# Performance work log

Hardware: AMD Instinct MI355X
Metric: run time of the kernel (lower is better)

Reference implementation:

```python
import jax, jax.numpy as jnp
import numpy as np

N_FEAT = 64
O_FEAT = 64
REDUCTION = 16


def conv2d(x, w, pad):
    # x: NCHW, w: OIHW
    return jax.lax.conv_general_dilated(
        x, w, window_strides=(1, 1), padding=[(pad, pad), (pad, pad)],
        dimension_numbers=('NCHW', 'OIHW', 'NCHW'))


def bwt(x):
    # Haar-like wavelet decompose: [B,C,H,W] -> [B,8C,H/2,W/2]
    x01 = x[:, :, 0::2, :] / 2
    x02 = x[:, :, 1::2, :] / 2
    x1 = x01[:, :, :, 0::2]
    x2 = x02[:, :, :, 0::2]
    x3 = x01[:, :, :, 1::2]
    x4 = x02[:, :, :, 1::2]
    x_LL = x1 + x2 + x3 + x4
    x_HL = -x1 - x2 + x3 + x4
    x_LH = -x1 + x2 - x3 + x4
    x_HH = x1 - x2 - x3 + x4
    x_HD = x1 + x2 - x3 - x4
    x_LV = -x1 + x2 + x3 - x4
    x_LD = x1 - x2 + x3 - x4
    x_HV = -x1 - x2 - x3 - x4
    return jnp.concatenate((x_LL, x_HL, x_LH, x_HH, x_HD, x_LV, x_LD, x_HV), axis=1)


def ibwt(x):
    # [B,8C,h,w] -> [B,C,2h,2w]
    B, C8, h, w = x.shape
    C = C8 // 8
    xs = [x[:, i * C:(i + 1) * C] / 2 for i in range(8)]
    x1, x2, x3, x4, x5, x6, x7, x8 = xs
    a00 = x1 - x2 - x3 + x4 + x5 - x6 + x7 - x8  # h[0::2, 0::2]
    a10 = x1 - x2 + x3 - x4 - x5 + x6 - x7 + x8  # h[1::2, 0::2]
    a01 = x1 + x2 - x3 - x4 - x5 - x6 + x7 + x8  # h[0::2, 1::2]
    a11 = x1 + x2 + x3 + x4 + x5 + x6 + x7 + x8  # h[1::2, 1::2]
    # interleave columns then rows
    even_rows = jnp.stack([a00, a01], axis=-1).reshape(B, C, h, 2 * w)
    odd_rows = jnp.stack([a10, a11], axis=-1).reshape(B, C, h, 2 * w)
    return jnp.stack([even_rows, odd_rows], axis=-2).reshape(B, C, 2 * h, 2 * w)


def sal(x, w_sal):
    max_pool = jnp.max(x, axis=1, keepdims=True)
    avg_pool = jnp.mean(x, axis=1, keepdims=True)
    channel_pool = jnp.concatenate([max_pool, avg_pool], axis=1)
    y = jax.nn.sigmoid(conv2d(channel_pool, w_sal, pad=2))
    return x * y


def cal(x, w_ca1, w_ca2):
    y = jnp.mean(x, axis=(2, 3), keepdims=True)  # adaptive avg pool to 1x1
    y = jax.nn.relu(conv2d(y, w_ca1, pad=0))
    y = jax.nn.sigmoid(conv2d(y, w_ca2, pad=0))
    return x * y


def setup_inputs() -> dict:
    key = jax.random.key(0)
    ks = jax.random.split(key, 10)
    n, o, r = N_FEAT, O_FEAT, REDUCTION
    s = 0.05
    return {
        'x': jax.random.normal(ks[0], (4, n, 256, 256), dtype=jnp.float32),
        'w_body1': jax.random.normal(ks[1], (n, 8 * n, 3, 3), dtype=jnp.float32) * s,
        'w_body2': jax.random.normal(ks[2], (8 * n, n, 3, 3), dtype=jnp.float32) * s,
        'w_sal': jax.random.normal(ks[3], (1, 2, 5, 5), dtype=jnp.float32) * s,
        'w_ca1': jax.random.normal(ks[4], (8 * n // r, 8 * n, 1, 1), dtype=jnp.float32) * s,
        'w_ca2': jax.random.normal(ks[5], (8 * n, 8 * n // r, 1, 1), dtype=jnp.float32) * s,
        'w_1x1': jax.random.normal(ks[6], (8 * n, 8 * n, 1, 1), dtype=jnp.float32) * s,
        'w_3x3': jax.random.normal(ks[7], (o, n, 3, 3), dtype=jnp.float32) * s,
        'w_final': jax.random.normal(ks[8], (o, n, 1, 1), dtype=jnp.float32) * s,
    }


def reference(x, w_body1, w_body2, w_sal, w_ca1, w_ca2, w_1x1, w_3x3, w_final):
    residual = x
    x_bwt = bwt(x)                               # [B, 8n, H/2, W/2]
    res = conv2d(x_bwt, w_body1, pad=1)          # body: conv-act-conv
    res = jax.nn.relu(res)
    res = conv2d(res, w_body2, pad=1)
    res = sal(res, w_sal)
    res = cal(res, w_ca1, w_ca2)
    res = conv2d(res, w_1x1, pad=0) + x_bwt
    wavelet_path = ibwt(res)                     # [B, n, H, W]
    out = jax.nn.relu(conv2d(wavelet_path, w_3x3, pad=1))
    out = out + conv2d(residual, w_final, pad=0)
    return out
```

## Files before the change

kernel.cpp:

```cpp
#include <hip/hip_runtime.h>
#include <hip/hip_bf16.h>

typedef __hip_bfloat16 bf16;
using short8  = __attribute__((ext_vector_type(8))) short;
using floatx4 = __attribute__((ext_vector_type(4))) float;

__device__ __forceinline__ float b2f(bf16 v) { return __bfloat162float(v); }
__device__ __forceinline__ bf16 f2b(float v) { return __float2bfloat16(v); }
__device__ __forceinline__ float s2f(short s) {
    return __uint_as_float(((unsigned)(unsigned short)s) << 16);
}

constexpr int Bz = 4, H = 256, W = 256, Hh = 128, Wh = 128, C8 = 512;
constexpr int HWh = Hh * Wh;
constexpr int HWf = H * W;
constexpr int ICP = 40;

template<int OC, int IC>
__global__ __launch_bounds__(256) void prep_wr(const float* __restrict__ w, bf16* __restrict__ wr) {
    int idx = blockIdx.x * 256 + threadIdx.x;
    if (idx >= 9 * OC * IC) return;
    int ic = idx & (IC - 1);
    int oc = (idx / IC) & (OC - 1);
    int tap = idx / (IC * OC);
    wr[idx] = f2b(w[(oc * IC + ic) * 9 + tap]);
}

__global__ __launch_bounds__(256) void prep_wfr(const float* __restrict__ wf, bf16* __restrict__ wfr) {
    int idx = blockIdx.x * 256 + threadIdx.x;
    wfr[idx] = f2b(wf[idx]);
}

__global__ __launch_bounds__(256) void prep_w1s(const float* __restrict__ w1,
                                                const float* __restrict__ scale,
                                                bf16* __restrict__ w1s) {
    int idx = blockIdx.x * 256 + threadIdx.x;
    int ic = idx & 511, oc = (idx >> 9) & 511, b = idx >> 18;
    w1s[idx] = f2b(w1[oc * 512 + ic] * scale[b * 512 + ic]);
}

__global__ __launch_bounds__(256) void bwt_nhwc(const float* __restrict__ x, bf16* __restrict__ A) {
    int idx = blockIdx.x * 256 + threadIdx.x;
    int c = idx & 63;
    int j = (idx >> 6) & 127;
    int i = (idx >> 13) & 127;
    int b = idx >> 20;
    const float* xp = x + ((size_t)(b * 64 + c) * H + 2 * i) * W + 2 * j;
    float2 ev = *(const float2*)xp;
    float2 od = *(const float2*)(xp + W);
    float x1 = ev.x * 0.5f, x3 = ev.y * 0.5f, x2 = od.x * 0.5f, x4 = od.y * 0.5f;
    float v[8];
    v[0] =  x1 + x2 + x3 + x4;
    v[1] = -x1 - x2 + x3 + x4;
    v[2] = -x1 + x2 - x3 + x4;
    v[3] =  x1 - x2 - x3 + x4;
    v[4] =  x1 + x2 - x3 - x4;
    v[5] = -x1 + x2 + x3 - x4;
    v[6] =  x1 - x2 + x3 - x4;
    v[7] = -x1 - x2 - x3 - x4;
    size_t base = (size_t)(idx >> 6) * 512 + c;
    #pragma unroll
    for (int k = 0; k < 8; k++)
        A[base + k * 64] = f2b(v[k]);
}

template<int IC, int OC, int HW, int TR, bool RELU>
__global__ __launch_bounds__(256, 2) void conv3x3_mfma(const bf16* __restrict__ in,
                                                       const bf16* __restrict__ wr,
                                                       bf16* __restrict__ out) {
    constexpr int MT = TR / 4;
    __shared__ bf16 sIn[(TR + 2) * 18 * ICP];
    __shared__ bf16 sW3[3 * 64 * ICP];

    const int tilesX = HW / 16;
    int tX = (blockIdx.x % tilesX) * 16;
    int tY = (blockIdx.x / tilesX) * TR;
    int oBase = blockIdx.y * 64;
    int b = blockIdx.z;
    int tid = threadIdx.x;
    int lane = tid & 63, wid = tid >> 6;
    int m = lane & 15, quad = lane >> 4;

    floatx4 acc[MT][4];
    #pragma unroll
    for (int i = 0; i < MT; i++)
        #pragma unroll
        for (int j = 0; j < 4; j++)
            acc[i][j] = (floatx4){0.f, 0.f, 0.f, 0.f};

    const bf16* inB = in + (size_t)b * HW * HW * IC;

    for (int ic0 = 0; ic0 < IC; ic0 += 32) {
        __syncthreads();
        for (int e = tid; e < (TR + 2) * 18 * 4; e += 256) {
            int q = e & 3, cell = e >> 2;
            int r = cell / 18, c = cell - r * 18;
            int gr = tY + r - 1, gc = tX + c - 1;
            short8 v = {0, 0, 0, 0, 0, 0, 0, 0};
            if (gr >= 0 && gr < HW && gc >= 0 && gc < HW)
                v = *(const short8*)(inB + (size_t)(gr * HW + gc) * IC + ic0 + q * 8);
            *(short8*)(sIn + cell * ICP + q * 8) = v;
        }
        for (int dy = 0; dy < 3; dy++) {
            if (dy) __syncthreads();
            for (int e = tid; e < 768; e += 256) {
                int q = e & 3, row = e >> 2;
                int dxl = row >> 6, oc = row & 63;
                int tap = dy * 3 + dxl;
                short8 v = *(const short8*)(wr + (size_t)(tap * OC + oBase + oc) * IC + ic0 + q * 8);
                *(short8*)(sW3 + row * ICP + q * 8) = v;
            }
            __syncthreads();
            #pragma unroll
            for (int dx = 0; dx < 3; dx++) {
                short8 bfr[4];
                #pragma unroll
                for (int nt = 0; nt < 4; nt++)
                    bfr[nt] = *(const short8*)(sW3 + (dx * 64 + nt * 16 + m) * ICP + quad * 8);
                #pragma unroll
                for (int mt = 0; mt < MT; mt++) {
                    int r = wid * MT + mt;
                    short8 afr = *(const short8*)(sIn + ((r + dy) * 18 + m + dx) * ICP + quad * 8);
                    #pragma unroll
                    for (int nt = 0; nt < 4; nt++)
                        acc[mt][nt] = __builtin_amdgcn_mfma_f32_16x16x32_bf16(afr, bfr[nt], acc[mt][nt], 0, 0, 0);
                }
            }
        }
    }
    #pragma unroll
    for (int mt = 0; mt < MT; mt++) {
        int row = tY + wid * MT + mt;
        #pragma unroll
        for (int nt = 0; nt < 4; nt++) {
            int oc = oBase + nt * 16 + m;
            #pragma unroll
            for (int reg = 0; reg < 4; reg++) {
                int col = tX + quad * 4 + reg;
                float v = acc[mt][nt][reg];
                if (RELU) v = fmaxf(v, 0.f);
                out[((size_t)(b * HW + row) * HW + col) * OC + oc] = f2b(v);
            }
        }
    }
}

__global__ __launch_bounds__(256, 2) void conv1x1_mfma(const bf16* __restrict__ t3,
                                                       const bf16* __restrict__ w1s,
                                                       bf16* __restrict__ A) {
    __shared__ bf16 sX[256 * ICP];
    __shared__ bf16 sW1[64 * ICP];
    int p0 = blockIdx.x * 256;
    int oBase = blockIdx.y * 64;
    int b = blockIdx.z;
    int tid = threadIdx.x;
    int lane = tid & 63, wid = tid >> 6;
    int m = lane & 15, quad = lane >> 4;
    const bf16* wB = w1s + (size_t)b * 512 * 512;
    const bf16* tB = t3 + ((size_t)b << 14) * 512;

    floatx4 acc[4][4];
    #pragma unroll
    for (int i = 0; i < 4; i++)
        #pragma unroll
        for (int j = 0; j < 4; j++)
            acc[i][j] = (floatx4){0.f, 0.f, 0.f, 0.f};

    for (int ic0 = 0; ic0 < 512; ic0 += 32) {
        __syncthreads();
        #pragma unroll
        for (int k = 0; k < 4; k++) {
            int e = tid + k * 256;
            int q = e & 3, p = e >> 2;
            *(short8*)(sX + p * ICP + q * 8) =
                *(const short8*)(tB + (size_t)(p0 + p) * 512 + ic0 + q * 8);
        }
        {
            int q = tid & 3, oc = tid >> 2;
            *(short8*)(sW1 + oc * ICP + q * 8) =
                *(const short8*)(wB + (size_t)(oBase + oc) * 512 + ic0 + q * 8);
        }
        __syncthreads();
        short8 bfr[4];
        #pragma unroll
        for (int nt = 0; nt < 4; nt++)
            bfr[nt] = *(const short8*)(sW1 + (nt * 16 + m) * ICP + quad * 8);
        #pragma unroll
        for (int mt = 0; mt < 4; mt++) {
            short8 afr = *(const short8*)(sX + ((wid * 4 + mt) * 16 + m) * ICP + quad * 8);
            #pragma unroll
            for (int nt = 0; nt < 4; nt++)
                acc[mt][nt] = __builtin_amdgcn_mfma_f32_16x16x32_bf16(afr, bfr[nt], acc[mt][nt], 0, 0, 0);
        }
    }
    bf16* AB = A + ((size_t)b << 14) * 512;
    #pragma unroll
    for (int mt = 0; mt < 4; mt++) {
        #pragma unroll
        for (int nt = 0; nt < 4; nt++) {
            int oc = oBase + nt * 16 + m;
            #pragma unroll
            for (int reg = 0; reg < 4; reg++) {
                int p = p0 + (wid * 4 + mt) * 16 + quad * 4 + reg;
                size_t a = (size_t)p * 512 + oc;
                AB[a] = f2b(acc[mt][nt][reg] + b2f(AB[a]));
            }
        }
    }
}

__global__ __launch_bounds__(256) void sal_pool(const bf16* __restrict__ t2, float* __restrict__ pool) {
    int pix = blockIdx.x * 4 + (threadIdx.x >> 6);
    int lane = threadIdx.x & 63;
    short8 v = *(const short8*)(t2 + (size_t)pix * 512 + lane * 8);
    float mx = -1e30f, sm = 0.f;
    #pragma unroll
    for (int i = 0; i < 8; i++) {
        float f = s2f(v[i]);
        mx = fmaxf(mx, f);
        sm += f;
    }
    #pragma unroll
    for (int off = 32; off > 0; off >>= 1) {
        mx = fmaxf(mx, __shfl_xor(mx, off));
        sm += __shfl_xor(sm, off);
    }
    if (lane == 0) {
        int b = pix >> 14, px = pix & (HWh - 1);
        pool[((size_t)(b * 2) << 14) + px] = mx;
        pool[((size_t)(b * 2 + 1) << 14) + px] = sm * (1.f / 512.f);
    }
}

__global__ __launch_bounds__(256) void sal_conv(const float* __restrict__ pool,
                                                const float* __restrict__ wsal,
                                                float* __restrict__ smap) {
    int p = blockIdx.x * 256 + threadIdx.x;
    int b = p >> 14, px = p & (HWh - 1);
    int iy = px >> 7, ix = px & 127;
    float acc = 0.f;
    #pragma unroll
    for (int ch = 0; ch < 2; ch++)
        #pragma unroll
        for (int dy = 0; dy < 5; dy++)
            #pragma unroll
            for (int dx = 0; dx < 5; dx++) {
                int gy = iy + dy - 2, gx = ix + dx - 2;
                if (gy >= 0 && gy < Hh && gx >= 0 && gx < Wh)
                    acc += pool[((size_t)(b * 2 + ch) << 14) + gy * Wh + gx] *
                           wsal[ch * 25 + dy * 5 + dx];
            }
    smap[p] = 1.f / (1.f + expf(-acc));
}

__global__ __launch_bounds__(256) void sal_mul_sum(bf16* __restrict__ t2,
                                                   const float* __restrict__ smap,
                                                   float* __restrict__ chsum) {
    int b = blockIdx.y;
    int p0 = blockIdx.x * 32;
    int t = threadIdx.x;
    float s0 = 0.f, s1 = 0.f;
    bf16* tB = t2 + ((size_t)b << 14) * 512;
    #pragma unroll 4
    for (int k = 0; k < 32; k++) {
        int pix = p0 + k;
        float sc = smap[(b << 14) + pix];
        size_t base = (size_t)pix * 512 + 2 * t;
        float f0 = b2f(tB[base]) * sc;
        float f1 = b2f(tB[base + 1]) * sc;
        tB[base] = f2b(f0);
        tB[base + 1] = f2b(f1);
        s0 += f0; s1 += f1;
    }
    atomicAdd(&chsum[b * 512 + 2 * t], s0);
    atomicAdd(&chsum[b * 512 + 2 * t + 1], s1);
}

__global__ __launch_bounds__(512) void cal_kernel(const float* __restrict__ chsum,
                                                  const float* __restrict__ wca1,
                                                  const float* __restrict__ wca2,
                                                  float* __restrict__ scale) {
    int b = blockIdx.x;
    __shared__ float sMean[512];
    __shared__ float sH[32];
    sMean[threadIdx.x] = chsum[b * C8 + threadIdx.x] * (1.f / 16384.f);
    __syncthreads();
    if (threadIdx.x < 32) {
        float a = 0.f;
        for (int cc = 0; cc < 512; cc++)
            a += wca1[threadIdx.x * 512 + cc] * sMean[cc];
        sH[threadIdx.x] = fmaxf(a, 0.f);
    }
    __syncthreads();
    float a = 0.f;
    #pragma unroll
    for (int j = 0; j < 32; j++)
        a += wca2[threadIdx.x * 32 + j] * sH[j];
    scale[b * C8 + threadIdx.x] = 1.f / (1.f + expf(-a));
}

__global__ __launch_bounds__(256) void ibwt_nhwc(const bf16* __restrict__ A, bf16* __restrict__ E) {
    int idx = blockIdx.x * 256 + threadIdx.x;
    int c = idx & 63;
    int j = (idx >> 6) & 127;
    int i = (idx >> 13) & 127;
    int b = idx >> 20;
    size_t base = (size_t)(idx >> 6) * 512 + c;
    float xs[8];
    #pragma unroll
    for (int k = 0; k < 8; k++)
        xs[k] = b2f(A[base + k * 64]) * 0.5f;
    float a00 = xs[0] - xs[1] - xs[2] + xs[3] + xs[4] - xs[5] + xs[6] - xs[7];
    float a10 = xs[0] - xs[1] + xs[2] - xs[3] - xs[4] + xs[5] - xs[6] + xs[7];
    float a01 = xs[0] + xs[1] - xs[2] - xs[3] - xs[4] - xs[5] + xs[6] + xs[7];
    float a11 = xs[0] + xs[1] + xs[2] + xs[3] + xs[4] + xs[5] + xs[6] + xs[7];
    bf16* Ep = E + ((size_t)((b * H + 2 * i) * W + 2 * j)) * 64 + c;
    Ep[0]          = f2b(a00);
    Ep[64]         = f2b(a01);
    Ep[W * 64]     = f2b(a10);
    Ep[W * 64 + 64] = f2b(a11);
}

__global__ __launch_bounds__(256, 2) void final_mfma(const bf16* __restrict__ E,
                                                     const bf16* __restrict__ wr3,
                                                     const float* __restrict__ x,
                                                     const bf16* __restrict__ wfr,
                                                     float* __restrict__ out) {
    __shared__ bf16 sIn[18 * 18 * ICP];
    __shared__ bf16 sW3[3 * 64 * ICP];
    const int tilesX = W / 16;
    int tX = (blockIdx.x % tilesX) * 16;
    int tY = (blockIdx.x / tilesX) * 16;
    int b = blockIdx.z;
    int tid = threadIdx.x;
    int lane = tid & 63, wid = tid >> 6;
    int m = lane & 15, quad = lane >> 4;

    floatx4 acc[4][4];
    #pragma unroll
    for (int i = 0; i < 4; i++)
        #pragma unroll
        for (int j = 0; j < 4; j++)
            acc[i][j] = (floatx4){0.f, 0.f, 0.f, 0.f};

    const bf16* inB = E + (size_t)b * HWf * 64;
    for (int ic0 = 0; ic0 < 64; ic0 += 32) {
        __syncthreads();
        for (int e = tid; e < 18 * 18 * 4; e += 256) {
            int q = e & 3, cell = e >> 2;
            int r = cell / 18, c = cell - r * 18;
            int gr = tY + r - 1, gc = tX + c - 1;
            short8 v = {0, 0, 0, 0, 0, 0, 0, 0};
            if (gr >= 0 && gr < H && gc >= 0 && gc < W)
                v = *(const short8*)(inB + (size_t)(gr * W + gc) * 64 + ic0 + q * 8);
            *(short8*)(sIn + cell * ICP + q * 8) = v;
        }
        for (int dy = 0; dy < 3; dy++) {
            if (dy) __syncthreads();
            for (int e = tid; e < 768; e += 256) {
                int q = e & 3, row = e >> 2;
                int dxl = row >> 6, oc = row & 63;
                int tap = dy * 3 + dxl;
                short8 v = *(const short8*)(wr3 + (size_t)(tap * 64 + oc) * 64 + ic0 + q * 8);
                *(short8*)(sW3 + row * ICP + q * 8) = v;
            }
            __syncthreads();
            #pragma unroll
            for (int dx = 0; dx < 3; dx++) {
                short8 bfr[4];
                #pragma unroll
                for (int nt = 0; nt < 4; nt++)
                    bfr[nt] = *(const short8*)(sW3 + (dx * 64 + nt * 16 + m) * ICP + quad * 8);
                #pragma unroll
                for (int mt = 0; mt < 4; mt++) {
                    int r = wid * 4 + mt;
                    short8 afr = *(const short8*)(sIn + ((r + dy) * 18 + m + dx) * ICP + quad * 8);
                    #pragma unroll
                    for (int nt = 0; nt < 4; nt++)
                        acc[mt][nt] = __builtin_amdgcn_mfma_f32_16x16x32_bf16(afr, bfr[nt], acc[mt][nt], 0, 0, 0);
                }
            }
        }
    }
    #pragma unroll
    for (int i = 0; i < 4; i++)
        #pragma unroll
        for (int j = 0; j < 4; j++)
            #pragma unroll
            for (int r = 0; r < 4; r++)
                acc[i][j][r] = fmaxf(acc[i][j][r], 0.f);

    for (int icc = 0; icc < 64; icc += 32) {
        __syncthreads();
        for (int e = tid; e < 2048; e += 256) {
            int c4 = e & 3, r = (e >> 2) & 15, ic = e >> 6;
            float4 v = *(const float4*)(x + ((size_t)(b * 64 + icc + ic) * H + tY + r) * W + tX + c4 * 4);
            bf16* dst = sIn + ((r + 1) * 18 + c4 * 4 + 1) * ICP + ic;
            dst[0]       = f2b(v.x);
            dst[ICP]     = f2b(v.y);
            dst[2 * ICP] = f2b(v.z);
            dst[3 * ICP] = f2b(v.w);
        }
        {
            int q = tid & 3, oc = tid >> 2;
            *(short8*)(sW3 + (64 + oc) * ICP + q * 8) =
                *(const short8*)(wfr + oc * 64 + icc + q * 8);
        }
        __syncthreads();
        short8 bfr[4];
        #pragma unroll
        for (int nt = 0; nt < 4; nt++)
            bfr[nt] = *(const short8*)(sW3 + (64 + nt * 16 + m) * ICP + quad * 8);
        #pragma unroll
        for (int mt = 0; mt < 4; mt++) {
            int r = wid * 4 + mt;
            short8 afr = *(const short8*)(sIn + ((r + 1) * 18 + m + 1) * ICP + quad * 8);
            #pragma unroll
            for (int nt = 0; nt < 4; nt++)
                acc[mt][nt] = __builtin_amdgcn_mfma_f32_16x16x32_bf16(afr, bfr[nt], acc[mt][nt], 0, 0, 0);
        }
    }
    #pragma unroll
    for (int mt = 0; mt < 4; mt++) {
        int gr = tY + wid * 4 + mt;
        #pragma unroll
        for (int nt = 0; nt < 4; nt++) {
            int oc = nt * 16 + m;
            *(floatx4*)(out + ((size_t)(b * 64 + oc) * H + gr) * W + tX + quad * 4) = acc[mt][nt];
        }
    }
}

extern "C" void kernel_launch(void* const* d_in, const int* in_sizes, int n_in,
                              void* d_out, int out_size, void* d_ws, size_t ws_size,
                              hipStream_t stream) {
    const float* x       = (const float*)d_in[0];
    const float* w_body1 = (const float*)d_in[1];
    const float* w_body2 = (const float*)d_in[2];
    const float* w_sal   = (const float*)d_in[3];
    const float* w_ca1   = (const float*)d_in[4];
    const float* w_ca2   = (const float*)d_in[5];
    const float* w_1x1   = (const float*)d_in[6];
    const float* w_3x3   = (const float*)d_in[7];
    const float* w_final = (const float*)d_in[8];

    char* ws = (char*)d_ws;
    bf16*  A     = (bf16*)(ws + 0);
    bf16*  T2    = (bf16*)(ws + 67108864);
    bf16*  T1    = (bf16*)(ws + 134217728);
    float* pool  = (float*)(ws + 134217728);
    float* smap  = (float*)(ws + 134742016);
    float* chsum = (float*)(ws + 135004160);
    float* scale = (float*)(ws + 135012352);
    bf16*  w1s   = (bf16*)(ws + 135020544);
    bf16*  wr3   = (bf16*)(ws + 137117696);
    bf16*  wfr   = (bf16*)(ws + 137191424);
    bf16*  E     = T2;
    bf16*  wr1   = (bf16*)d_out;
    bf16*  wr2   = (bf16*)((char*)d_out + 589824);

    prep_wr<64, 512><<<1152, 256, 0, stream>>>(w_body1, wr1);
    prep_wr<512, 64><<<1152, 256, 0, stream>>>(w_body2, wr2);
    bwt_nhwc<<<16384, 256, 0, stream>>>(x, A);
    conv3x3_mfma<512, 64, 128, 8, true ><<<dim3(128, 1, 4), 256, 0, stream>>>(A, wr1, T1);
    conv3x3_mfma<64, 512, 128, 16, false><<<dim3(64, 8, 4), 256, 0, stream>>>(T1, wr2, T2);
    sal_pool<<<16384, 256, 0, stream>>>(T2, pool);
    sal_conv<<<256, 256, 0, stream>>>(pool, w_sal, smap);
    hipMemsetAsync(chsum, 0, 4 * 512 * sizeof(float), stream);
    sal_mul_sum<<<dim3(512, 4), 256, 0, stream>>>(T2, smap, chsum);
    cal_kernel<<<4, 512, 0, stream>>>(chsum, w_ca1, w_ca2, scale);
    prep_w1s<<<4096, 256, 0, stream>>>(w_1x1, scale, w1s);
    prep_wr<64, 64><<<144, 256, 0, stream>>>(w_3x3, wr3);
    prep_wfr<<<16, 256, 0, stream>>>(w_final, wfr);
    conv1x1_mfma<<<dim3(64, 8, 4), 256, 0, stream>>>(T2, w1s, A);
    ibwt_nhwc<<<16384, 256, 0, stream>>>(A, E);
    final_mfma<<<dim3(256, 1, 4), 256, 0, stream>>>(E, wr3, x, wfr, (float*)d_out);
}
```

Measured before the change: 521.9 us.

## Fuse spatial-attention scaling into 1x1 conv, restage weights, tile bwt via LDS

The spatial-attention multiply no longer writes back into T2. sal_wsum only accumulates the weighted channel sums, and the smap scaling is applied while T2 is staged into shared memory inside conv1x1, which also widens its output tile to 128 channels. The 3x3 convs and final kernel load all nine tap weights per input-channel chunk with one barrier instead of three, and the first conv uses 16-row tiles with launch bound 1. bwt now stages coalesced float4 reads through LDS, rounding x to bf16 before the transform. This cuts one full read-modify-write pass over T2 and some synchronisation, at the cost of more LDS and registers, lower occupancy and fewer blocks for conv1.

```diff
diff --git a/kernel.cpp b/kernel.cpp
--- a/kernel.cpp
+++ b/kernel.cpp
@@ -10,8 +10,12 @@
 __device__ __forceinline__ float s2f(short s) {
     return __uint_as_float(((unsigned)(unsigned short)s) << 16);
 }
-
-constexpr int Bz = 4, H = 256, W = 256, Hh = 128, Wh = 128, C8 = 512;
+__device__ __forceinline__ unsigned short fbits(float v) {
+    bf16 b = f2b(v);
+    return *(unsigned short*)&b;
+}
+
+constexpr int H = 256, W = 256, Hh = 128, Wh = 128, C8 = 512;
 constexpr int HWh = Hh * Wh;
 constexpr int HWf = H * W;
 constexpr int ICP = 40;
@@ -39,51 +43,68 @@
     w1s[idx] = f2b(w1[oc * 512 + ic] * scale[b * 512 + ic]);
 }
 
-__global__ __launch_bounds__(256) void bwt_nhwc(const float* __restrict__ x, bf16* __restrict__ A) {
-    int idx = blockIdx.x * 256 + threadIdx.x;
-    int c = idx & 63;
-    int j = (idx >> 6) & 127;
-    int i = (idx >> 13) & 127;
-    int b = idx >> 20;
-    const float* xp = x + ((size_t)(b * 64 + c) * H + 2 * i) * W + 2 * j;
-    float2 ev = *(const float2*)xp;
-    float2 od = *(const float2*)(xp + W);
-    float x1 = ev.x * 0.5f, x3 = ev.y * 0.5f, x2 = od.x * 0.5f, x4 = od.y * 0.5f;
-    float v[8];
-    v[0] =  x1 + x2 + x3 + x4;
-    v[1] = -x1 - x2 + x3 + x4;
-    v[2] = -x1 + x2 - x3 + x4;
-    v[3] =  x1 - x2 - x3 + x4;
-    v[4] =  x1 + x2 - x3 - x4;
-    v[5] = -x1 + x2 + x3 - x4;
-    v[6] =  x1 - x2 + x3 - x4;
-    v[7] = -x1 - x2 - x3 - x4;
-    size_t base = (size_t)(idx >> 6) * 512 + c;
-    #pragma unroll
-    for (int k = 0; k < 8; k++)
-        A[base + k * 64] = f2b(v[k]);
-}
-
-template<int IC, int OC, int HW, int TR, bool RELU>
-__global__ __launch_bounds__(256, 2) void conv3x3_mfma(const bf16* __restrict__ in,
-                                                       const bf16* __restrict__ wr,
-                                                       bf16* __restrict__ out) {
-    constexpr int MT = TR / 4;
-    __shared__ bf16 sIn[(TR + 2) * 18 * ICP];
-    __shared__ bf16 sW3[3 * 64 * ICP];
+constexpr int XROW = 130;
+__global__ __launch_bounds__(256, 2) void bwt_nhwc(const float* __restrict__ x, bf16* __restrict__ A) {
+    __shared__ unsigned short sX[2 * 64 * XROW];
+    int bx = blockIdx.x;
+    int i = bx >> 1, j0 = (bx & 1) * 64;
+    int b = blockIdx.z;
+    int tid = threadIdx.x;
+    for (int k = 0; k < 16; k++) {
+        int e = tid + k * 256;
+        int w4 = e & 31, r = (e >> 5) & 1, c = e >> 6;
+        float4 v = *(const float4*)(x + (((size_t)(b * 64 + c) * H + 2 * i + r) * W) + j0 * 2 + w4 * 4);
+        unsigned lo = ((unsigned)fbits(v.y) << 16) | fbits(v.x);
+        unsigned hi = ((unsigned)fbits(v.w) << 16) | fbits(v.z);
+        unsigned short* dst = sX + (r * 64 + c) * XROW + w4 * 4;
+        *(unsigned*)(dst) = lo;
+        *(unsigned*)(dst + 2) = hi;
+    }
+    __syncthreads();
+    int c = tid & 63, wid = tid >> 6;
+    for (int k = 0; k < 16; k++) {
+        int jr = wid * 16 + k;
+        unsigned ev = *(const unsigned*)(sX + c * XROW + jr * 2);
+        unsigned od = *(const unsigned*)(sX + (64 + c) * XROW + jr * 2);
+        float x1 = s2f((short)(ev & 0xffff)) * 0.5f;
+        float x3 = s2f((short)(ev >> 16)) * 0.5f;
+        float x2 = s2f((short)(od & 0xffff)) * 0.5f;
+        float x4 = s2f((short)(od >> 16)) * 0.5f;
+        float v[8];
+        v[0] =  x1 + x2 + x3 + x4;
+        v[1] = -x1 - x2 + x3 + x4;
+        v[2] = -x1 + x2 - x3 + x4;
+        v[3] =  x1 - x2 - x3 + x4;
+        v[4] =  x1 + x2 - x3 - x4;
+        v[5] = -x1 + x2 + x3 - x4;
+        v[6] =  x1 - x2 + x3 - x4;
+        v[7] = -x1 - x2 - x3 - x4;
+        size_t base = ((size_t)((b * Hh + i) * Wh) + j0 + jr) * 512 + c;
+        #pragma unroll
+        for (int band = 0; band < 8; band++)
+            A[base + band * 64] = f2b(v[band]);
+    }
+}
+
+template<int IC, int OC, int HW, bool RELU, int MINW>
+__global__ __launch_bounds__(256, MINW) void conv3x3_mfma(const bf16* __restrict__ in,
+                                                          const bf16* __restrict__ wr,
+                                                          bf16* __restrict__ out) {
+    __shared__ bf16 sIn[18 * 18 * ICP];
+    __shared__ bf16 sW9[9 * 64 * ICP];
 
     const int tilesX = HW / 16;
     int tX = (blockIdx.x % tilesX) * 16;
-    int tY = (blockIdx.x / tilesX) * TR;
+    int tY = (blockIdx.x / tilesX) * 16;
     int oBase = blockIdx.y * 64;
     int b = blockIdx.z;
     int tid = threadIdx.x;
     int lane = tid & 63, wid = tid >> 6;
     int m = lane & 15, quad = lane >> 4;
 
-    floatx4 acc[MT][4];
-    #pragma unroll
-    for (int i = 0; i < MT; i++)
+    floatx4 acc[4][4];
+    #pragma unroll
+    for (int i = 0; i < 4; i++)
         #pragma unroll
         for (int j = 0; j < 4; j++)
             acc[i][j] = (floatx4){0.f, 0.f, 0.f, 0.f};
@@ -92,7 +113,7 @@
 
     for (int ic0 = 0; ic0 < IC; ic0 += 32) {
         __syncthreads();
-        for (int e = tid; e < (TR + 2) * 18 * 4; e += 256) {
+        for (int e = tid; e < 18 * 18 * 4; e += 256) {
             int q = e & 3, cell = e >> 2;
             int r = cell / 18, c = cell - r * 18;
             int gr = tY + r - 1, gc = tX + c - 1;
@@ -101,25 +122,24 @@
                 v = *(const short8*)(inB + (size_t)(gr * HW + gc) * IC + ic0 + q * 8);
             *(short8*)(sIn + cell * ICP + q * 8) = v;
         }
+        for (int e = tid; e < 2304; e += 256) {
+            int q = e & 3, row = e >> 2;
+            int tap = row >> 6, oc = row & 63;
+            short8 v = *(const short8*)(wr + (size_t)(tap * OC + oBase + oc) * IC + ic0 + q * 8);
+            *(short8*)(sW9 + row * ICP + q * 8) = v;
+        }
+        __syncthreads();
+        #pragma unroll
         for (int dy = 0; dy < 3; dy++) {
-            if (dy) __syncthreads();
-            for (int e = tid; e < 768; e += 256) {
-                int q = e & 3, row = e >> 2;
-                int dxl = row >> 6, oc = row & 63;
-                int tap = dy * 3 + dxl;
-                short8 v = *(const short8*)(wr + (size_t)(tap * OC + oBase + oc) * IC + ic0 + q * 8);
-                *(short8*)(sW3 + row * ICP + q * 8) = v;
-            }
-            __syncthreads();
             #pragma unroll
             for (int dx = 0; dx < 3; dx++) {
                 short8 bfr[4];
                 #pragma unroll
                 for (int nt = 0; nt < 4; nt++)
-                    bfr[nt] = *(const short8*)(sW3 + (dx * 64 + nt * 16 + m) * ICP + quad * 8);
+                    bfr[nt] = *(const short8*)(sW9 + ((dy * 3 + dx) * 64 + nt * 16 + m) * ICP + quad * 8);
                 #pragma unroll
-                for (int mt = 0; mt < MT; mt++) {
-                    int r = wid * MT + mt;
+                for (int mt = 0; mt < 4; mt++) {
+                    int r = wid * 4 + mt;
                     short8 afr = *(const short8*)(sIn + ((r + dy) * 18 + m + dx) * ICP + quad * 8);
                     #pragma unroll
                     for (int nt = 0; nt < 4; nt++)
@@ -129,8 +149,8 @@
         }
     }
     #pragma unroll
-    for (int mt = 0; mt < MT; mt++) {
-        int row = tY + wid * MT + mt;
+    for (int mt = 0; mt < 4; mt++) {
+        int row = tY + wid * 4 + mt;
         #pragma unroll
         for (int nt = 0; nt < 4; nt++) {
             int oc = oBase + nt * 16 + m;
@@ -146,24 +166,26 @@
 }
 
 __global__ __launch_bounds__(256, 2) void conv1x1_mfma(const bf16* __restrict__ t3,
+                                                       const float* __restrict__ smap,
                                                        const bf16* __restrict__ w1s,
                                                        bf16* __restrict__ A) {
     __shared__ bf16 sX[256 * ICP];
-    __shared__ bf16 sW1[64 * ICP];
+    __shared__ bf16 sW1[128 * ICP];
     int p0 = blockIdx.x * 256;
-    int oBase = blockIdx.y * 64;
+    int oBase = blockIdx.y * 128;
     int b = blockIdx.z;
     int tid = threadIdx.x;
     int lane = tid & 63, wid = tid >> 6;
     int m = lane & 15, quad = lane >> 4;
     const bf16* wB = w1s + (size_t)b * 512 * 512;
     const bf16* tB = t3 + ((size_t)b << 14) * 512;
-
-    floatx4 acc[4][4];
+    const float* sm = smap + (b << 14);
+
+    floatx4 acc[4][8];
     #pragma unroll
     for (int i = 0; i < 4; i++)
         #pragma unroll
-        for (int j = 0; j < 4; j++)
+        for (int j = 0; j < 8; j++)
             acc[i][j] = (floatx4){0.f, 0.f, 0.f, 0.f};
 
     for (int ic0 = 0; ic0 < 512; ic0 += 32) {
@@ -172,24 +194,31 @@
         for (int k = 0; k < 4; k++) {
             int e = tid + k * 256;
             int q = e & 3, p = e >> 2;
-            *(short8*)(sX + p * ICP + q * 8) =
-                *(const short8*)(tB + (size_t)(p0 + p) * 512 + ic0 + q * 8);
-        }
-        {
-            int q = tid & 3, oc = tid >> 2;
+            float sc = sm[p0 + p];
+            short8 v = *(const short8*)(tB + (size_t)(p0 + p) * 512 + ic0 + q * 8);
+            short8 o;
+            #pragma unroll
+            for (int t = 0; t < 8; t++)
+                o[t] = (short)fbits(s2f(v[t]) * sc);
+            *(short8*)(sX + p * ICP + q * 8) = o;
+        }
+        #pragma unroll
+        for (int k = 0; k < 2; k++) {
+            int e = tid + k * 256;
+            int q = e & 3, oc = e >> 2;
             *(short8*)(sW1 + oc * ICP + q * 8) =
                 *(const short8*)(wB + (size_t)(oBase + oc) * 512 + ic0 + q * 8);
         }
         __syncthreads();
-        short8 bfr[4];
-        #pragma unroll
-        for (int nt = 0; nt < 4; nt++)
+        short8 bfr[8];
+        #pragma unroll
+        for (int nt = 0; nt < 8; nt++)
             bfr[nt] = *(const short8*)(sW1 + (nt * 16 + m) * ICP + quad * 8);
         #pragma unroll
         for (int mt = 0; mt < 4; mt++) {
             short8 afr = *(const short8*)(sX + ((wid * 4 + mt) * 16 + m) * ICP + quad * 8);
             #pragma unroll
-            for (int nt = 0; nt < 4; nt++)
+            for (int nt = 0; nt < 8; nt++)
                 acc[mt][nt] = __builtin_amdgcn_mfma_f32_16x16x32_bf16(afr, bfr[nt], acc[mt][nt], 0, 0, 0);
         }
     }
@@ -197,11 +226,11 @@
     #pragma unroll
     for (int mt = 0; mt < 4; mt++) {
         #pragma unroll
-        for (int nt = 0; nt < 4; nt++) {
+        for (int nt = 0; nt < 8; nt++) {
             int oc = oBase + nt * 16 + m;
             #pragma unroll
             for (int reg = 0; reg < 4; reg++) {
-                int p = p0 + (wid * 4 + mt) * 16 + quad * 4 + reg;
+                int p = p0 + wid * 64 + mt * 16 + quad * 4 + reg;
                 size_t a = (size_t)p * 512 + oc;
                 AB[a] = f2b(acc[mt][nt][reg] + b2f(AB[a]));
             }
@@ -253,24 +282,21 @@
     smap[p] = 1.f / (1.f + expf(-acc));
 }
 
-__global__ __launch_bounds__(256) void sal_mul_sum(bf16* __restrict__ t2,
-                                                   const float* __restrict__ smap,
-                                                   float* __restrict__ chsum) {
+__global__ __launch_bounds__(256) void sal_wsum(const bf16* __restrict__ t2,
+                                                const float* __restrict__ smap,
+                                                float* __restrict__ chsum) {
     int b = blockIdx.y;
     int p0 = blockIdx.x * 32;
     int t = threadIdx.x;
     float s0 = 0.f, s1 = 0.f;
-    bf16* tB = t2 + ((size_t)b << 14) * 512;
+    const bf16* tB = t2 + ((size_t)b << 14) * 512;
     #pragma unroll 4
     for (int k = 0; k < 32; k++) {
         int pix = p0 + k;
         float sc = smap[(b << 14) + pix];
-        size_t base = (size_t)pix * 512 + 2 * t;
-        float f0 = b2f(tB[base]) * sc;
-        float f1 = b2f(tB[base + 1]) * sc;
-        tB[base] = f2b(f0);
-        tB[base + 1] = f2b(f1);
-        s0 += f0; s1 += f1;
+        unsigned v = *(const unsigned*)(tB + (size_t)pix * 512 + 2 * t);
+        s0 += s2f((short)(v & 0xffff)) * sc;
+        s1 += s2f((short)(v >> 16)) * sc;
     }
     atomicAdd(&chsum[b * 512 + 2 * t], s0);
     atomicAdd(&chsum[b * 512 + 2 * t + 1], s1);
@@ -315,9 +341,9 @@
     float a01 = xs[0] + xs[1] - xs[2] - xs[3] - xs[4] - xs[5] + xs[6] + xs[7];
     float a11 = xs[0] + xs[1] + xs[2] + xs[3] + xs[4] + xs[5] + xs[6] + xs[7];
     bf16* Ep = E + ((size_t)((b * H + 2 * i) * W + 2 * j)) * 64 + c;
-    Ep[0]          = f2b(a00);
-    Ep[64]         = f2b(a01);
-    Ep[W * 64]     = f2b(a10);
+    Ep[0]           = f2b(a00);
+    Ep[64]          = f2b(a01);
+    Ep[W * 64]      = f2b(a10);
     Ep[W * 64 + 64] = f2b(a11);
 }
 
@@ -327,7 +353,7 @@
                                                      const bf16* __restrict__ wfr,
                                                      float* __restrict__ out) {
     __shared__ bf16 sIn[18 * 18 * ICP];
-    __shared__ bf16 sW3[3 * 64 * ICP];
+    __shared__ bf16 sW9[9 * 64 * ICP];
     const int tilesX = W / 16;
     int tX = (blockIdx.x % tilesX) * 16;
     int tY = (blockIdx.x / tilesX) * 16;
@@ -355,22 +381,21 @@
                 v = *(const short8*)(inB + (size_t)(gr * W + gc) * 64 + ic0 + q * 8);
             *(short8*)(sIn + cell * ICP + q * 8) = v;
         }
+        for (int e = tid; e < 2304; e += 256) {
+            int q = e & 3, row = e >> 2;
+            int tap = row >> 6, oc = row & 63;
+            short8 v = *(const short8*)(wr3 + (size_t)(tap * 64 + oc) * 64 + ic0 + q * 8);
+            *(short8*)(sW9 + row * ICP + q * 8) = v;
+        }
+        __syncthreads();
+        #pragma unroll
         for (int dy = 0; dy < 3; dy++) {
-            if (dy) __syncthreads();
-            for (int e = tid; e < 768; e += 256) {
-                int q = e & 3, row = e >> 2;
-                int dxl = row >> 6, oc = row & 63;
-                int tap = dy * 3 + dxl;
-                short8 v = *(const short8*)(wr3 + (size_t)(tap * 64 + oc) * 64 + ic0 + q * 8);
-                *(short8*)(sW3 + row * ICP + q * 8) = v;
-            }
-            __syncthreads();
             #pragma unroll
             for (int dx = 0; dx < 3; dx++) {
                 short8 bfr[4];
                 #pragma unroll
                 for (int nt = 0; nt < 4; nt++)
-                    bfr[nt] = *(const short8*)(sW3 + (dx * 64 + nt * 16 + m) * ICP + quad * 8);
+                    bfr[nt] = *(const short8*)(sW9 + ((dy * 3 + dx) * 64 + nt * 16 + m) * ICP + quad * 8);
                 #pragma unroll
                 for (int mt = 0; mt < 4; mt++) {
                     int r = wid * 4 + mt;
@@ -403,14 +428,14 @@
         }
         {
             int q = tid & 3, oc = tid >> 2;
-            *(short8*)(sW3 + (64 + oc) * ICP + q * 8) =
+            *(short8*)(sW9 + (64 + oc) * ICP + q * 8) =
                 *(const short8*)(wfr + oc * 64 + icc + q * 8);
         }
         __syncthreads();
         short8 bfr[4];
         #pragma unroll
         for (int nt = 0; nt < 4; nt++)
-            bfr[nt] = *(const short8*)(sW3 + (64 + nt * 16 + m) * ICP + quad * 8);
+            bfr[nt] = *(const short8*)(sW9 + (64 + nt * 16 + m) * ICP + quad * 8);
         #pragma unroll
         for (int mt = 0; mt < 4; mt++) {
             int r = wid * 4 + mt;
@@ -461,18 +486,18 @@
 
     prep_wr<64, 512><<<1152, 256, 0, stream>>>(w_body1, wr1);
     prep_wr<512, 64><<<1152, 256, 0, stream>>>(w_body2, wr2);
-    bwt_nhwc<<<16384, 256, 0, stream>>>(x, A);
-    conv3x3_mfma<512, 64, 128, 8, true ><<<dim3(128, 1, 4), 256, 0, stream>>>(A, wr1, T1);
-    conv3x3_mfma<64, 512, 128, 16, false><<<dim3(64, 8, 4), 256, 0, stream>>>(T1, wr2, T2);
+    bwt_nhwc<<<dim3(256, 1, 4), 256, 0, stream>>>(x, A);
+    conv3x3_mfma<512, 64, 128, true, 1><<<dim3(64, 1, 4), 256, 0, stream>>>(A, wr1, T1);
+    conv3x3_mfma<64, 512, 128, false, 2><<<dim3(64, 8, 4), 256, 0, stream>>>(T1, wr2, T2);
     sal_pool<<<16384, 256, 0, stream>>>(T2, pool);
     sal_conv<<<256, 256, 0, stream>>>(pool, w_sal, smap);
     hipMemsetAsync(chsum, 0, 4 * 512 * sizeof(float), stream);
-    sal_mul_sum<<<dim3(512, 4), 256, 0, stream>>>(T2, smap, chsum);
+    sal_wsum<<<dim3(512, 4), 256, 0, stream>>>(T2, smap, chsum);
     cal_kernel<<<4, 512, 0, stream>>>(chsum, w_ca1, w_ca2, scale);
     prep_w1s<<<4096, 256, 0, stream>>>(w_1x1, scale, w1s);
     prep_wr<64, 64><<<144, 256, 0, stream>>>(w_3x3, wr3);
     prep_wfr<<<16, 256, 0, stream>>>(w_final, wfr);
-    conv1x1_mfma<<<dim3(64, 8, 4), 256, 0, stream>>>(T2, w1s, A);
+    conv1x1_mfma<<<dim3(64, 4, 4), 256, 0, stream>>>(T2, smap, w1s, A);
     ibwt_nhwc<<<16384, 256, 0, stream>>>(A, E);
     final_mfma<<<dim3(256, 1, 4), 256, 0, stream>>>(E, wr3, x, wfr, (float*)d_out);
 }
```

Result: faster. 478.7 us (-8.3%).
